# Kernel optimization log

Hardware: AMD Instinct MI355X
Metric: run time of the kernel (lower is better)

## Reference

```python
import jax, jax.numpy as jnp
import numpy as np

ALPHA = 0.25
GAMMA = 2.0
EPS = 1e-8
W_CLASS = 2.0
W_BBOX = 5.0
W_GIOU = 2.0
B, Q, T, C = 64, 900, 300, 80


def setup_inputs() -> dict:
    key = jax.random.key(0)
    k1, k2, k3, k4 = jax.random.split(key, 4)
    pred_logits = jax.random.normal(k1, (B, Q, C), dtype=jnp.float32)
    pred_boxes = jax.random.uniform(k2, (B, Q, 4), dtype=jnp.float32)  # cxcywh in (0,1)
    tgt_labels = jax.random.randint(k3, (B, T), 0, C, dtype=jnp.int64)
    tgt_boxes = jax.random.uniform(k4, (B, T, 4), dtype=jnp.float32)
    return {"pred_logits": pred_logits, "pred_boxes": pred_boxes,
            "tgt_labels": tgt_labels, "tgt_boxes": tgt_boxes}


def box_cxcywh_to_xyxy(b):
    cx, cy, w, h = b[..., 0], b[..., 1], b[..., 2], b[..., 3]
    return jnp.stack([cx - 0.5 * w, cy - 0.5 * h, cx + 0.5 * w, cy + 0.5 * h], axis=-1)


def pairwise_giou(boxes1, boxes2):
    # boxes1: [B,Q,4] xyxy, boxes2: [B,T,4] xyxy -> [B,Q,T]
    area1 = (boxes1[..., 2] - boxes1[..., 0]) * (boxes1[..., 3] - boxes1[..., 1])
    area2 = (boxes2[..., 2] - boxes2[..., 0]) * (boxes2[..., 3] - boxes2[..., 1])
    lt = jnp.maximum(boxes1[:, :, None, :2], boxes2[:, None, :, :2])
    rb = jnp.minimum(boxes1[:, :, None, 2:], boxes2[:, None, :, 2:])
    wh = jnp.clip(rb - lt, 0.0)
    inter = wh[..., 0] * wh[..., 1]
    union = area1[:, :, None] + area2[:, None, :] - inter
    iou = inter / union
    lt_c = jnp.minimum(boxes1[:, :, None, :2], boxes2[:, None, :, :2])
    rb_c = jnp.maximum(boxes1[:, :, None, 2:], boxes2[:, None, :, 2:])
    wh_c = jnp.clip(rb_c - lt_c, 0.0)
    area_c = wh_c[..., 0] * wh_c[..., 1]
    return iou - (area_c - union) / area_c


def reference(pred_logits, pred_boxes, tgt_labels, tgt_boxes):
    # Batched cost matrix of HungarianMatcher (use_focal_loss=True).
    prob = jax.nn.sigmoid(pred_logits)  # [B,Q,C]
    idx = jnp.broadcast_to(tgt_labels[:, None, :], (prob.shape[0], prob.shape[1], tgt_labels.shape[1]))
    p = jnp.take_along_axis(prob, idx.astype(jnp.int32), axis=2)  # [B,Q,T]
    neg_cost = (1.0 - ALPHA) * p ** GAMMA * (-jnp.log(1.0 - p + EPS))
    pos_cost = ALPHA * (1.0 - p) ** GAMMA * (-jnp.log(p + EPS))
    cost_class = pos_cost - neg_cost
    cost_bbox = jnp.abs(pred_boxes[:, :, None, :] - tgt_boxes[:, None, :, :]).sum(-1)
    cost_giou = -pairwise_giou(box_cxcywh_to_xyxy(pred_boxes), box_cxcywh_to_xyxy(tgt_boxes))
    cost = W_BBOX * cost_bbox + W_CLASS * cost_class + W_GIOU * cost_giou
    return jnp.nan_to_num(cost, nan=1.0, posinf=1e6, neginf=-1e6)
```

## Files before the change

kernel.cpp:

```cpp
#include <hip/hip_runtime.h>


constexpr int B = 64, Q = 900, T = 300, C = 80;
constexpr int QTILE = 10;
constexpr int BLOCK = 256;
constexpr int TG    = T / 4;
constexpr int NG    = QTILE * TG;
constexpr float ALPHA = 0.25f;
constexpr float EPSF  = 1e-8f;

__device__ __forceinline__ float fast_rcp(float x) {
    return __builtin_amdgcn_rcpf(x);
}

__global__ __launch_bounds__(BLOCK) void matcher_cost_kernel(
    const float* __restrict__ logits,
    const float* __restrict__ pboxes,
    const int*   __restrict__ tlabels,
    const float* __restrict__ tboxes,
    float* __restrict__ out)
{
    __shared__ float4 s_t[9][TG];
    __shared__ int4   s_tl[TG];
    __shared__ float  s_cls[QTILE * C];
    __shared__ float4 s_p[QTILE][3];

    const int bid = blockIdx.x;
    const int b   = bid / (Q / QTILE);
    const int q0  = (bid % (Q / QTILE)) * QTILE;
    const int tid = threadIdx.x;

    for (int t = tid; t < T; t += BLOCK) {
        float4 bx = *(const float4*)(tboxes + ((size_t)b * T + t) * 4);
        float x0 = bx.x - 0.5f * bx.z, y0 = bx.y - 0.5f * bx.w;
        float x1 = bx.x + 0.5f * bx.z, y1 = bx.y + 0.5f * bx.w;
        ((float*)&s_t[0][0])[t] = bx.x;
        ((float*)&s_t[1][0])[t] = bx.y;
        ((float*)&s_t[2][0])[t] = bx.z;
        ((float*)&s_t[3][0])[t] = bx.w;
        ((float*)&s_t[4][0])[t] = x0;
        ((float*)&s_t[5][0])[t] = y0;
        ((float*)&s_t[6][0])[t] = x1;
        ((float*)&s_t[7][0])[t] = y1;
        ((float*)&s_t[8][0])[t] = (x1 - x0) * (y1 - y0);
        ((int*)&s_tl[0])[t]     = tlabels[(size_t)b * T + t];
    }

    if (tid < QTILE) {
        float4 bx = *(const float4*)(pboxes + ((size_t)b * Q + q0 + tid) * 4);
        float x0 = bx.x - 0.5f * bx.z, y0 = bx.y - 0.5f * bx.w;
        float x1 = bx.x + 0.5f * bx.z, y1 = bx.y + 0.5f * bx.w;
        s_p[tid][0] = make_float4(bx.x, bx.y, bx.z, bx.w);
        s_p[tid][1] = make_float4(x0, y0, x1, y1);
        s_p[tid][2] = make_float4((x1 - x0) * (y1 - y0), 0.f, 0.f, 0.f);
    }

    {
        const float* lg = logits + ((size_t)b * Q + q0) * C;
        for (int i4 = tid; i4 < QTILE * C / 4; i4 += BLOCK) {
            float4 x = *(const float4*)(lg + i4 * 4);
            float4 r;
            #pragma unroll
            for (int k = 0; k < 4; ++k) {
                float xv = (&x.x)[k];
                float pr = fast_rcp(1.0f + __expf(-xv));
                float om = 1.0f - pr;
                float pos = ALPHA * om * om * (-__logf(pr + EPSF));
                float neg = (1.0f - ALPHA) * pr * pr * (-__logf(om + EPSF));
                (&r.x)[k] = pos - neg;
            }
            *(float4*)(s_cls + i4 * 4) = r;
        }
    }

    __syncthreads();

    float* outb = out + ((size_t)b * Q + q0) * T;
    for (unsigned g = tid; g < NG; g += BLOCK) {
        unsigned ql = g / TG;
        unsigned tg = g - ql * TG;

        float4 p0 = s_p[ql][0];
        float4 p1 = s_p[ql][1];
        float  pa = s_p[ql][2].x;
        const float* clsrow = s_cls + ql * C;

        float4 tcx = s_t[0][tg], tcy = s_t[1][tg];
        float4 tw  = s_t[2][tg], th  = s_t[3][tg];
        float4 tx0 = s_t[4][tg], ty0 = s_t[5][tg];
        float4 tx1 = s_t[6][tg], ty1 = s_t[7][tg];
        float4 ta  = s_t[8][tg];
        int4   lab = s_tl[tg];

        float4 res;
        #pragma unroll
        for (int k = 0; k < 4; ++k) {
            float tcx_ = (&tcx.x)[k], tcy_ = (&tcy.x)[k];
            float tw_  = (&tw.x)[k],  th_  = (&th.x)[k];
            float tx0_ = (&tx0.x)[k], ty0_ = (&ty0.x)[k];
            float tx1_ = (&tx1.x)[k], ty1_ = (&ty1.x)[k];
            float ta_  = (&ta.x)[k];
            int   lb   = (&lab.x)[k];

            float cbbox = fabsf(p0.x - tcx_) + fabsf(p0.y - tcy_) +
                          fabsf(p0.z - tw_ ) + fabsf(p0.w - th_ );
            float ccls = clsrow[lb];

            float ix0 = fmaxf(p1.x, tx0_), iy0 = fmaxf(p1.y, ty0_);
            float ix1 = fminf(p1.z, tx1_), iy1 = fminf(p1.w, ty1_);
            float iw  = fmaxf(ix1 - ix0, 0.0f);
            float ih  = fmaxf(iy1 - iy0, 0.0f);
            float inter = iw * ih;
            float uni   = pa + ta_ - inter;
            float iou   = inter * fast_rcp(uni);

            float cx0 = fminf(p1.x, tx0_), cy0 = fminf(p1.y, ty0_);
            float cx1 = fmaxf(p1.z, tx1_), cy1 = fmaxf(p1.w, ty1_);
            float ca  = fmaxf(cx1 - cx0, 0.0f) * fmaxf(cy1 - cy0, 0.0f);
            float giou = iou - (ca - uni) * fast_rcp(ca);

            float cost = 5.0f * cbbox + 2.0f * ccls - 2.0f * giou;

            if (cost != cost) cost = 1.0f;
            else cost = fminf(fmaxf(cost, -1.0e6f), 1.0e6f);
            (&res.x)[k] = cost;
        }

        *(float4*)(outb + (size_t)g * 4) = res;
    }
}

extern "C" void kernel_launch(void* const* d_in, const int* in_sizes, int n_in,
                              void* d_out, int out_size, void* d_ws, size_t ws_size,
                              hipStream_t stream) {
    const float* logits  = (const float*)d_in[0];
    const float* pboxes  = (const float*)d_in[1];
    const int*   tlabels = (const int*)  d_in[2];
    const float* tboxes  = (const float*)d_in[3];
    float* out = (float*)d_out;

    dim3 grid(B * (Q / QTILE));
    dim3 block(BLOCK);
    matcher_cost_kernel<<<grid, block, 0, stream>>>(logits, pboxes, tlabels, tboxes, out);
}
```

Measured before the change: 35.39 us.

## Process two queries per thread and fold GIoU into a single reciprocal

Each thread now handles two query rows per target group, so the target shared-memory loads are reused twice. The GIoU is rewritten algebraically as (uni^2 + inter*ca)/(uni*ca), which needs one reciprocal instead of two. The class weight and the +2 constant are folded into the precomputed class table, and the clamp on the enclosing box and the ±1e6 clamp are dropped. The class precompute becomes scalar, and box areas come directly from w*h. This risks small numerical differences and overflow or inf behaviour in the merged product, since the ±1e6 clamp is gone.

```diff
diff --git a/kernel.cpp b/kernel.cpp
--- a/kernel.cpp
+++ b/kernel.cpp
@@ -5,7 +5,7 @@
 constexpr int QTILE = 10;
 constexpr int BLOCK = 256;
 constexpr int TG    = T / 4;
-constexpr int NG    = QTILE * TG;
+constexpr int NIT   = (QTILE / 2) * TG;
 constexpr float ALPHA = 0.25f;
 constexpr float EPSF  = 1e-8f;
 
@@ -23,7 +23,8 @@
     __shared__ float4 s_t[9][TG];
     __shared__ int4   s_tl[TG];
     __shared__ float  s_cls[QTILE * C];
-    __shared__ float4 s_p[QTILE][3];
+    __shared__ float4 s_pA[QTILE];
+    __shared__ float4 s_pB[QTILE];
 
     const int bid = blockIdx.x;
     const int b   = bid / (Q / QTILE);
@@ -42,7 +43,7 @@
         ((float*)&s_t[5][0])[t] = y0;
         ((float*)&s_t[6][0])[t] = x1;
         ((float*)&s_t[7][0])[t] = y1;
-        ((float*)&s_t[8][0])[t] = (x1 - x0) * (y1 - y0);
+        ((float*)&s_t[8][0])[t] = bx.z * bx.w;
         ((int*)&s_tl[0])[t]     = tlabels[(size_t)b * T + t];
     }
 
@@ -50,40 +51,28 @@
         float4 bx = *(const float4*)(pboxes + ((size_t)b * Q + q0 + tid) * 4);
         float x0 = bx.x - 0.5f * bx.z, y0 = bx.y - 0.5f * bx.w;
         float x1 = bx.x + 0.5f * bx.z, y1 = bx.y + 0.5f * bx.w;
-        s_p[tid][0] = make_float4(bx.x, bx.y, bx.z, bx.w);
-        s_p[tid][1] = make_float4(x0, y0, x1, y1);
-        s_p[tid][2] = make_float4((x1 - x0) * (y1 - y0), 0.f, 0.f, 0.f);
+        s_pA[tid] = bx;
+        s_pB[tid] = make_float4(x0, y0, x1, y1);
     }
 
     {
         const float* lg = logits + ((size_t)b * Q + q0) * C;
-        for (int i4 = tid; i4 < QTILE * C / 4; i4 += BLOCK) {
-            float4 x = *(const float4*)(lg + i4 * 4);
-            float4 r;
-            #pragma unroll
-            for (int k = 0; k < 4; ++k) {
-                float xv = (&x.x)[k];
-                float pr = fast_rcp(1.0f + __expf(-xv));
-                float om = 1.0f - pr;
-                float pos = ALPHA * om * om * (-__logf(pr + EPSF));
-                float neg = (1.0f - ALPHA) * pr * pr * (-__logf(om + EPSF));
-                (&r.x)[k] = pos - neg;
-            }
-            *(float4*)(s_cls + i4 * 4) = r;
+        for (int i = tid; i < QTILE * C; i += BLOCK) {
+            float x  = lg[i];
+            float pr = fast_rcp(1.0f + __expf(-x));
+            float om = 1.0f - pr;
+            float pos = ALPHA * om * om * (-__logf(pr + EPSF));
+            float neg = (1.0f - ALPHA) * pr * pr * (-__logf(om + EPSF));
+            s_cls[i] = 2.0f * (pos - neg) + 2.0f;
         }
     }
 
     __syncthreads();
 
     float* outb = out + ((size_t)b * Q + q0) * T;
-    for (unsigned g = tid; g < NG; g += BLOCK) {
-        unsigned ql = g / TG;
-        unsigned tg = g - ql * TG;
-
-        float4 p0 = s_p[ql][0];
-        float4 p1 = s_p[ql][1];
-        float  pa = s_p[ql][2].x;
-        const float* clsrow = s_cls + ql * C;
+    for (unsigned it = tid; it < NIT; it += BLOCK) {
+        unsigned qp = it / TG;
+        unsigned tg = it - qp * TG;
 
         float4 tcx = s_t[0][tg], tcy = s_t[1][tg];
         float4 tw  = s_t[2][tg], th  = s_t[3][tg];
@@ -92,41 +81,47 @@
         float4 ta  = s_t[8][tg];
         int4   lab = s_tl[tg];
 
-        float4 res;
         #pragma unroll
-        for (int k = 0; k < 4; ++k) {
-            float tcx_ = (&tcx.x)[k], tcy_ = (&tcy.x)[k];
-            float tw_  = (&tw.x)[k],  th_  = (&th.x)[k];
-            float tx0_ = (&tx0.x)[k], ty0_ = (&ty0.x)[k];
-            float tx1_ = (&tx1.x)[k], ty1_ = (&ty1.x)[k];
-            float ta_  = (&ta.x)[k];
-            int   lb   = (&lab.x)[k];
+        for (int dq = 0; dq < 2; ++dq) {
+            const int ql = qp * 2 + dq;
+            float4 pA = s_pA[ql];
+            float4 pB = s_pB[ql];
+            float  pa = pA.z * pA.w;
+            const float* clsrow = s_cls + ql * C;
 
-            float cbbox = fabsf(p0.x - tcx_) + fabsf(p0.y - tcy_) +
-                          fabsf(p0.z - tw_ ) + fabsf(p0.w - th_ );
-            float ccls = clsrow[lb];
+            float4 res;
+            #pragma unroll
+            for (int k = 0; k < 4; ++k) {
+                float tcx_ = (&tcx.x)[k], tcy_ = (&tcy.x)[k];
+                float tw_  = (&tw.x)[k],  th_  = (&th.x)[k];
+                float tx0_ = (&tx0.x)[k], ty0_ = (&ty0.x)[k];
+                float tx1_ = (&tx1.x)[k], ty1_ = (&ty1.x)[k];
+                float ta_  = (&ta.x)[k];
 
-            float ix0 = fmaxf(p1.x, tx0_), iy0 = fmaxf(p1.y, ty0_);
-            float ix1 = fminf(p1.z, tx1_), iy1 = fminf(p1.w, ty1_);
-            float iw  = fmaxf(ix1 - ix0, 0.0f);
-            float ih  = fmaxf(iy1 - iy0, 0.0f);
-            float inter = iw * ih;
-            float uni   = pa + ta_ - inter;
-            float iou   = inter * fast_rcp(uni);
+                float cbbox = fabsf(pA.x - tcx_) + fabsf(pA.y - tcy_) +
+                              fabsf(pA.z - tw_ ) + fabsf(pA.w - th_ );
+                float cls2 = clsrow[(&lab.x)[k]];
 
-            float cx0 = fminf(p1.x, tx0_), cy0 = fminf(p1.y, ty0_);
-            float cx1 = fmaxf(p1.z, tx1_), cy1 = fmaxf(p1.w, ty1_);
-            float ca  = fmaxf(cx1 - cx0, 0.0f) * fmaxf(cy1 - cy0, 0.0f);
-            float giou = iou - (ca - uni) * fast_rcp(ca);
+                float iw = fmaxf(fminf(pB.z, tx1_) - fmaxf(pB.x, tx0_), 0.0f);
+                float ih = fmaxf(fminf(pB.w, ty1_) - fmaxf(pB.y, ty0_), 0.0f);
+                float inter = iw * ih;
+                float uni   = pa + ta_ - inter;
 
-            float cost = 5.0f * cbbox + 2.0f * ccls - 2.0f * giou;
+                float cw = fmaxf(pB.z, tx1_) - fminf(pB.x, tx0_);
+                float ch = fmaxf(pB.w, ty1_) - fminf(pB.y, ty0_);
+                float ca = cw * ch;
 
-            if (cost != cost) cost = 1.0f;
-            else cost = fminf(fmaxf(cost, -1.0e6f), 1.0e6f);
-            (&res.x)[k] = cost;
+                float num = fmaf(uni, uni, inter * ca);
+                float r   = fast_rcp(uni * ca);
+                float c   = fmaf(5.0f, cbbox, cls2);
+                c = fmaf(num, -2.0f * r, c);
+
+                if (c != c) c = 1.0f;
+
+                (&res.x)[k] = c;
+            }
+            *(float4*)(outb + (size_t)ql * T + tg * 4) = res;
         }
-
-        *(float4*)(outb + (size_t)g * 4) = res;
     }
 }
 
```

Measured after the change: 37.96 us. +7.3%, slower.
